# Performance work log

Measured on AMD Instinct MI355X. Metric: run time of the kernel, lower is better.

Reference implementation:

```python
import jax, jax.numpy as jnp
import numpy as np

B, S, DQK, DV, H = 4, 2048, 128, 128, 8


def setup_inputs() -> dict:
    key = jax.random.key(0)
    ks = jax.random.split(key, 9)
    s = 0.02
    return {
        "query": jax.random.normal(ks[0], (B, S, DQK), jnp.float32),
        "key": jax.random.normal(ks[1], (B, S, DQK), jnp.float32),
        "value": jax.random.normal(ks[2], (B, S, DV), jnp.float32),
        "WQ": jax.random.normal(ks[3], (DQK, H * DQK), jnp.float32) * s,
        "bQ": jax.random.normal(ks[4], (H * DQK,), jnp.float32) * s,
        "WK": jax.random.normal(ks[5], (DQK, H * DQK), jnp.float32) * s,
        "bK": jax.random.normal(ks[6], (H * DQK,), jnp.float32) * s,
        "WV": jax.random.normal(ks[7], (DV, H * DV), jnp.float32) * s,
        "bV": jax.random.normal(ks[8], (H * DV,), jnp.float32) * s,
    }


def reference(query, key, value, WQ, bQ, WK, bK, WV, bV):
    b, qn, dqk = query.shape
    kn = key.shape[1]
    dv = value.shape[2]
    h = H
    # projections -> [b, n, h, d]
    Q = (query @ WQ + bQ).reshape(b, qn, h, dqk)
    K = (key @ WK + bK).reshape(b, kn, h, dqk)
    V = (value @ WV + bV).reshape(b, kn, h, dv)
    # abs(QK^T)/sqrt(dk) score -- non-standard, prevents flash kernels
    scores = jnp.abs(jnp.einsum("bqhd,bkhd->bhqk", Q, K)) / jnp.sqrt(
        jnp.asarray(dqk, query.dtype)
    )
    w = jax.nn.softmax(scores, axis=-1)  # [b,h,q,k]
    # (complex cast +0j in the original is numerically a no-op on real V)
    out = jnp.einsum("bhqk,bkhd->bqhd", w, V).reshape(b, qn, h * dv)
    return out
```

## Files before the change

kernel.cpp:

```cpp
#include <hip/hip_runtime.h>
#include <hip/hip_bf16.h>

#define B_ 4
#define S_ 2048
#define D_ 128
#define H_ 8

typedef __attribute__((ext_vector_type(8))) short bf16x8;
typedef __attribute__((ext_vector_type(4))) float f32x4;

__device__ __forceinline__ short f2bf(float f) {
  union { float f; unsigned u; } v; v.f = f;
  unsigned u = v.u;
  unsigned r = (u + 0x7FFFu + ((u >> 16) & 1u)) >> 16;
  return (short)r;
}

__device__ __forceinline__ short4 pack4(f32x4 p) {
  union { __hip_bfloat162 h2[2]; short4 s4; } u;
  u.h2[0] = __float22bfloat162_rn(make_float2(p[0], p[1]));
  u.h2[1] = __float22bfloat162_rn(make_float2(p[2], p[3]));
  return u.s4;
}

__device__ __forceinline__ void dma16(const short* g, short* l) {
  __builtin_amdgcn_global_load_lds(
      (const __attribute__((address_space(1))) unsigned int*)g,
      (__attribute__((address_space(3))) unsigned int*)l, 16, 0, 0);
}

__global__ __launch_bounds__(256) void prep(
    const float* __restrict__ WQ, const float* __restrict__ WK, const float* __restrict__ WV,
    short* __restrict__ FQ, short* __restrict__ FK, short* __restrict__ FV) {
  __shared__ float tile[64][65];
  int bw = blockIdx.x >> 5;
  int tl = blockIdx.x & 31;
  int n0 = (tl & 15) * 64, k0 = (tl >> 4) * 64;
  const float* W = (bw == 0) ? WQ : (bw == 1) ? WK : WV;
  short* WF = (bw == 0) ? FQ : (bw == 1) ? FK : FV;
#pragma unroll
  for (int i = 0; i < 16; ++i) {
    int cix = threadIdx.x + 256 * i;
    int rr = cix >> 6, cc = cix & 63;
    tile[rr][cc] = W[(k0 + rr) * 1024 + n0 + cc];
  }
  __syncthreads();
#pragma unroll
  for (int i = 0; i < 16; ++i) {
    int cix = threadIdx.x + 256 * i;
    int rr = cix >> 6, cc = cix & 63;
    int n = n0 + rr, k = k0 + cc;
    size_t off = (size_t)(n >> 7) * 16384
               + (size_t)(((n >> 4) & 7) * 4 + (k >> 5)) * 512
               + ((k >> 3) & 3) * 128 + (n & 15) * 8 + (k & 7);
    WF[off] = f2bf(tile[cc][rr]);
  }
}

template <int MODE>
__device__ __forceinline__ void proj_pair(const float* __restrict__ X,
                                          const short* __restrict__ WF,
                                          const float* __restrict__ bias,
                                          short* __restrict__ out,
                                          int mtile, int np, short* sA) {
  int tid = threadIdx.x;
  int lane = tid & 63, w = tid >> 6;
  int l15 = lane & 15, l4 = lane >> 4;
  int m0 = mtile * 128;
  int bb = m0 >> 11;
  int mloc = m0 & 2047;

#pragma unroll
  for (int j = 0; j < 8; ++j) {
    int f = w * 8 + j;
    const float* src = X + (size_t)(m0 + (f >> 2) * 16 + l15) * 128 + (f & 3) * 32 + l4 * 8;
    float4 v0 = *(const float4*)src;
    float4 v1 = *(const float4*)(src + 4);
    union { struct { short4 lo, hi; } s; bf16x8 v; } u;
    u.s.lo = pack4((f32x4){v0.x, v0.y, v0.z, v0.w});
    u.s.hi = pack4((f32x4){v1.x, v1.y, v1.z, v1.w});
    *(bf16x8*)(sA + f * 512 + lane * 8) = u.v;
  }

  int wr = w >> 1, wc = w & 1;

  __syncthreads();

  bf16x8 a[4][4];
#pragma unroll
  for (int mi = 0; mi < 4; ++mi)
#pragma unroll
    for (int st = 0; st < 4; ++st)
      a[mi][st] = *(const bf16x8*)(sA + ((wr * 4 + mi) * 4 + st) * 512 + lane * 8);

#pragma unroll
  for (int nt = 0; nt < 2; ++nt) {
    int ntile = np * 2 + nt;
    int n0 = ntile * 128;

    const short* wfb = WF + (size_t)ntile * 16384 + wc * 8192 + lane * 8;

    f32x4 acc[4][4];
#pragma unroll
    for (int mi = 0; mi < 4; ++mi)
#pragma unroll
      for (int ni = 0; ni < 4; ++ni) acc[mi][ni] = (f32x4){0.f, 0.f, 0.f, 0.f};

#pragma unroll
    for (int ni = 0; ni < 4; ++ni) {
      bf16x8 bfr[4];
#pragma unroll
      for (int st = 0; st < 4; ++st)
        bfr[st] = *(const bf16x8*)(wfb + (ni * 4 + st) * 512);
#pragma unroll
      for (int mi = 0; mi < 4; ++mi) {
#pragma unroll
        for (int st = 0; st < 4; ++st) {
          if (MODE <= 1)
            acc[mi][ni] = __builtin_amdgcn_mfma_f32_16x16x32_bf16(bfr[st], a[mi][st], acc[mi][ni], 0, 0, 0);
          else
            acc[mi][ni] = __builtin_amdgcn_mfma_f32_16x16x32_bf16(a[mi][st], bfr[st], acc[mi][ni], 0, 0, 0);
        }
      }
    }

    __syncthreads();

    if (MODE == 0) {
#pragma unroll
      for (int mi = 0; mi < 4; ++mi) {
        int lrow = wr * 64 + mi * 16 + l15;
#pragma unroll
        for (int ni = 0; ni < 4; ++ni) {
          int d0 = wc * 64 + ni * 16 + l4 * 4;
          float4 bv = *(const float4*)(bias + n0 + d0);
          f32x4 t = acc[mi][ni];
          t[0] += bv.x; t[1] += bv.y; t[2] += bv.z; t[3] += bv.w;
          *(short4*)(sA + lrow * 128 + d0) = pack4(t);
        }
      }
    } else if (MODE == 1) {
#pragma unroll
      for (int mi = 0; mi < 4; ++mi) {
        int lk = wr * 64 + mi * 16 + l15;
        int kbase = (lk >> 6) * 8192 + ((lk >> 4) & 3) * 2048 + (lk & 15) * 8;
#pragma unroll
        for (int ni = 0; ni < 4; ++ni) {
          int d0 = wc * 64 + ni * 16 + l4 * 4;
          float4 bv = *(const float4*)(bias + n0 + d0);
          f32x4 t = acc[mi][ni];
          t[0] += bv.x; t[1] += bv.y; t[2] += bv.z; t[3] += bv.w;
          *(short4*)(sA + kbase + (d0 >> 5) * 512 + ((d0 >> 3) & 3) * 128 + (d0 & 7)) = pack4(t);
        }
      }
    } else {
#pragma unroll
      for (int ni = 0; ni < 4; ++ni) {
        int d = wc * 64 + ni * 16 + l15;
        float bvs = bias[n0 + d];
#pragma unroll
        for (int mi = 0; mi < 4; ++mi) {
          int ls0 = wr * 64 + mi * 16 + l4 * 4;
          f32x4 t = acc[mi][ni];
          t[0] += bvs; t[1] += bvs; t[2] += bvs; t[3] += bvs;
          *(short4*)(sA + (ls0 >> 6) * 8192
                        + ((d >> 4) * 2 + ((ls0 >> 5) & 1)) * 512
                        + ((ls0 >> 3) & 3) * 128 + (d & 15) * 8
                        + (ls0 & 7)) = pack4(t);
        }
      }
    }
    __syncthreads();

    short* gdst;
    if (MODE == 0)
      gdst = out + ((size_t)(bb * H_ + ntile) * S_ + mloc) * D_;
    else
      gdst = out + (size_t)(bb * H_ + ntile) * (S_ * D_) + (size_t)(mloc >> 6) * 8192;
#pragma unroll
    for (int i = 0; i < 8; ++i) {
      bf16x8 vv = *(const bf16x8*)(sA + (i * 256 + tid) * 8);
      *(bf16x8*)(gdst + (i * 256 + tid) * 8) = vv;
    }
  }
}

__global__ __launch_bounds__(256, 3) void proj3(
    const float* __restrict__ xq, const float* __restrict__ xk, const float* __restrict__ xv,
    const short* __restrict__ wtq, const short* __restrict__ wtk, const short* __restrict__ wtv,
    const float* __restrict__ bQ, const float* __restrict__ bK, const float* __restrict__ bV,
    short* __restrict__ Qp, short* __restrict__ Kf, short* __restrict__ Vf) {
  __shared__ short sA[16384];
  int work = (blockIdx.x & 7) * 96 + (blockIdx.x >> 3);
  int which = work >> 8;
  int t = work & 255;
  int mtile = t >> 2, np = t & 3;
  if (which == 0)      proj_pair<0>(xq, wtq, bQ, Qp, mtile, np, sA);
  else if (which == 1) proj_pair<1>(xk, wtk, bK, Kf, mtile, np, sA);
  else                 proj_pair<2>(xv, wtv, bV, Vf, mtile, np, sA);
}

#define PSTR 72

#define QK_H(KR)                                                               \
  _Pragma("unroll") for (int m = 0; m < 2; ++m) {                              \
    s0[m] = (f32x4){0.f, 0.f, 0.f, 0.f};                                       \
    s1[m] = (f32x4){0.f, 0.f, 0.f, 0.f};                                       \
    _Pragma("unroll") for (int st = 0; st < 4; ++st) {                         \
      s0[m] = __builtin_amdgcn_mfma_f32_16x16x32_bf16(KR[m * 4 + st], aq[0][st], s0[m], 0, 0, 0); \
      s1[m] = __builtin_amdgcn_mfma_f32_16x16x32_bf16(KR[m * 4 + st], aq[1][st], s1[m], 0, 0, 0); \
    }                                                                          \
  }

#define SM_H()                                                                 \
  _Pragma("unroll") for (int m = 0; m < 2; ++m) {                              \
    _Pragma("unroll") for (int r = 0; r < 4; ++r) {                            \
      float p = __builtin_amdgcn_exp2f(fabsf(s0[m][r]) * SC2);                 \
      ls0 += p;                                                                \
      s0[m][r] = p;                                                            \
    }                                                                          \
    *(short4*)(pw0 + l15 * PSTR + m * 16 + l4 * 4) = pack4(s0[m]);             \
  }                                                                            \
  _Pragma("unroll") for (int m = 0; m < 2; ++m) {                              \
    _Pragma("unroll") for (int r = 0; r < 4; ++r) {                            \
      float p = __builtin_amdgcn_exp2f(fabsf(s1[m][r]) * SC2);                 \
      ls1 += p;                                                                \
      s1[m][r] = p;                                                            \
    }                                                                          \
    *(short4*)(pw1 + l15 * PSTR + m * 16 + l4 * 4) = pack4(s1[m]);             \
  }                                                                            \
  ap0 = *(const bf16x8*)(pw0 + l15 * PSTR + l4 * 8);                           \
  ap1 = *(const bf16x8*)(pw1 + l15 * PSTR + l4 * 8);

#define PV_H()                                                                 \
  _Pragma("unroll") for (int t8 = 0; t8 < 8; ++t8) {                           \
    o0[t8] = __builtin_amdgcn_mfma_f32_16x16x32_bf16(ap0, bv[t8], o0[t8], 0, 0, 0); \
    o1[t8] = __builtin_amdgcn_mfma_f32_16x16x32_bf16(ap1, bv[t8], o1[t8], 0, 0, 0); \
  }

__global__ __launch_bounds__(512, 2) void attn(const short* __restrict__ Qp,
                                               const short* __restrict__ Kf,
                                               const short* __restrict__ Vf,
                                               float* __restrict__ out) {
  __shared__ short sK0[8192], sK1[8192];
  __shared__ short sV0[8192], sV1[8192];
  __shared__ short sP[16 * 16 * PSTR];

  int tid = threadIdx.x;
  int lane = tid & 63, w = tid >> 6;
  int xcd = blockIdx.x & 7;
  int idx = blockIdx.x >> 3;
  int bh  = xcd * 4 + (idx & 3);
  int qt  = idx >> 2;
  int q0  = qt * 256;
  int l15 = lane & 15, l4 = lane >> 4;

  const short* Qbase = Qp + (size_t)bh * S_ * D_;
  const short* kgs = Kf + (size_t)bh * S_ * D_ + 2 * w * 512 + lane * 8;
  const short* vgs = Vf + (size_t)bh * S_ * D_ + 2 * w * 512 + lane * 8;

  dma16(kgs,       sK0 + 2 * w * 512);
  dma16(kgs + 512, sK0 + (2 * w + 1) * 512);
  dma16(vgs,       sV0 + 2 * w * 512);
  dma16(vgs + 512, sV0 + (2 * w + 1) * 512);

  bf16x8 aq[2][4];
#pragma unroll
  for (int g = 0; g < 2; ++g)
#pragma unroll
    for (int st = 0; st < 4; ++st)
      aq[g][st] = *(const bf16x8*)(Qbase + (q0 + w * 32 + g * 16 + l15) * D_ + l4 * 8 + 32 * st);

  f32x4 o0[8], o1[8];
#pragma unroll
  for (int t = 0; t < 8; ++t) {
    o0[t] = (f32x4){0.f, 0.f, 0.f, 0.f};
    o1[t] = (f32x4){0.f, 0.f, 0.f, 0.f};
  }
  float ls0 = 0.f, ls1 = 0.f;

  const float SC2 = 0.127530637f;
  short* pw0 = sP + w * 16 * PSTR;
  short* pw1 = sP + (8 + w) * 16 * PSTR;

  __syncthreads();

  for (int t = 0; t < 32; ++t) {
    const short* sKc = (t & 1) ? sK1 : sK0;
    const short* sVc = (t & 1) ? sV1 : sV0;
    if (t < 31) {
      short* sKn = (t & 1) ? sK0 : sK1;
      short* sVn = (t & 1) ? sV0 : sV1;
      const short* kn = kgs + (size_t)(t + 1) * 8192;
      const short* vn = vgs + (size_t)(t + 1) * 8192;
      dma16(kn,       sKn + 2 * w * 512);
      dma16(kn + 512, sKn + (2 * w + 1) * 512);
      dma16(vn,       sVn + 2 * w * 512);
      dma16(vn + 512, sVn + (2 * w + 1) * 512);
    }
    bf16x8 kA[8], kB[8], bv[8];
#pragma unroll
    for (int j = 0; j < 8; ++j)
      kA[j] = *(const bf16x8*)(sKc + j * 512 + lane * 8);
#pragma unroll
    for (int j = 0; j < 8; ++j)
      kB[j] = *(const bf16x8*)(sKc + 4096 + j * 512 + lane * 8);
#pragma unroll
    for (int j = 0; j < 8; ++j)
      bv[j] = *(const bf16x8*)(sVc + (2 * j) * 512 + lane * 8);
    __builtin_amdgcn_sched_barrier(0);

    f32x4 s0[2], s1[2];
    bf16x8 ap0, ap1;
    __builtin_amdgcn_s_setprio(1);
    QK_H(kA);
    __builtin_amdgcn_s_setprio(0);
    SM_H();
    __builtin_amdgcn_s_setprio(1);
    PV_H();
    __builtin_amdgcn_s_setprio(0);
#pragma unroll
    for (int j = 0; j < 8; ++j)
      bv[j] = *(const bf16x8*)(sVc + (2 * j + 1) * 512 + lane * 8);
    __builtin_amdgcn_s_setprio(1);
    QK_H(kB);
    __builtin_amdgcn_s_setprio(0);
    SM_H();
    __builtin_amdgcn_s_setprio(1);
    PV_H();
    __builtin_amdgcn_s_setprio(0);
    __syncthreads();
  }

  ls0 += __shfl_xor(ls0, 16);
  ls0 += __shfl_xor(ls0, 32);
  ls1 += __shfl_xor(ls1, 16);
  ls1 += __shfl_xor(ls1, 32);
  float inv0[4], inv1[4];
#pragma unroll
  for (int r = 0; r < 4; ++r) {
    inv0[r] = 1.f / __shfl(ls0, l4 * 4 + r);
    inv1[r] = 1.f / __shfl(ls1, l4 * 4 + r);
  }

  int bb = bh >> 3, h = bh & 7;
#pragma unroll
  for (int t = 0; t < 8; ++t) {
#pragma unroll
    for (int r = 0; r < 4; ++r) {
      int qA = q0 + w * 32 + l4 * 4 + r;
      int qB = qA + 16;
      out[((size_t)(bb * S_ + qA)) * (H_ * D_) + h * D_ + t * 16 + l15] = o0[t][r] * inv0[r];
      out[((size_t)(bb * S_ + qB)) * (H_ * D_) + h * D_ + t * 16 + l15] = o1[t][r] * inv1[r];
    }
  }
}

extern "C" void kernel_launch(void* const* d_in, const int* in_sizes, int n_in,
                              void* d_out, int out_size, void* d_ws, size_t ws_size,
                              hipStream_t stream) {
  (void)in_sizes; (void)n_in; (void)out_size; (void)ws_size;
  const float* q  = (const float*)d_in[0];
  const float* k  = (const float*)d_in[1];
  const float* v  = (const float*)d_in[2];
  const float* WQ = (const float*)d_in[3];
  const float* bQ = (const float*)d_in[4];
  const float* WK = (const float*)d_in[5];
  const float* bK = (const float*)d_in[6];
  const float* WV = (const float*)d_in[7];
  const float* bV = (const float*)d_in[8];

  const int NW = D_ * H_ * D_;
  const int NP = B_ * H_ * S_ * D_;

  short* ws  = (short*)d_ws;
  short* wtq = ws;
  short* wtk = wtq + NW;
  short* wtv = wtk + NW;
  short* Qp  = wtv + NW;
  short* Kf  = Qp + NP;
  short* Vf  = Kf + NP;

  prep<<<96, 256, 0, stream>>>(WQ, WK, WV, wtq, wtk, wtv);

  proj3<<<768, 256, 0, stream>>>(q, k, v, wtq, wtk, wtv, bQ, bK, bV, Qp, Kf, Vf);

  attn<<<256, 512, 0, stream>>>(Qp, Kf, Vf, (float*)d_out);
}
```

Baseline: 176.2 us.

## Transpose softmax P tile via lane shuffles and halve attention block size

The probability tile is now rearranged from the MFMA accumulator layout into the A-operand layout with cross-lane shuffles, replacing the round trip through a shared-memory staging buffer. The attention kernel also moves to 256-thread blocks covering 128 queries each, launching twice as many blocks, with each wave issuing twice as many K/V DMA copies per tile. This removes LDS traffic and the shared P buffer and lowers per-block LDS use, but adds shuffle instructions and doubles total K/V loads across blocks.

```diff
diff --git a/kernel.cpp b/kernel.cpp
--- a/kernel.cpp
+++ b/kernel.cpp
@@ -200,8 +200,6 @@
   else                 proj_pair<2>(xv, wtv, bV, Vf, mtile, np, sA);
 }
 
-#define PSTR 72
-
 #define QK_H(KR)                                                               \
   _Pragma("unroll") for (int m = 0; m < 2; ++m) {                              \
     s0[m] = (f32x4){0.f, 0.f, 0.f, 0.f};                                       \
@@ -212,25 +210,30 @@
     }                                                                          \
   }
 
-#define SM_H()                                                                 \
-  _Pragma("unroll") for (int m = 0; m < 2; ++m) {                              \
-    _Pragma("unroll") for (int r = 0; r < 4; ++r) {                            \
-      float p = __builtin_amdgcn_exp2f(fabsf(s0[m][r]) * SC2);                 \
-      ls0 += p;                                                                \
-      s0[m][r] = p;                                                            \
+#define SM_X(S, LS, AP)                                                        \
+  {                                                                            \
+    _Pragma("unroll") for (int m = 0; m < 2; ++m) {                            \
+      _Pragma("unroll") for (int r = 0; r < 4; ++r) {                          \
+        float p = __builtin_amdgcn_exp2f(fabsf(S[m][r]) * SC2);                \
+        LS += p;                                                               \
+        S[m][r] = p;                                                           \
+      }                                                                        \
     }                                                                          \
-    *(short4*)(pw0 + l15 * PSTR + m * 16 + l4 * 4) = pack4(s0[m]);             \
-  }                                                                            \
-  _Pragma("unroll") for (int m = 0; m < 2; ++m) {                              \
-    _Pragma("unroll") for (int r = 0; r < 4; ++r) {                            \
-      float p = __builtin_amdgcn_exp2f(fabsf(s1[m][r]) * SC2);                 \
-      ls1 += p;                                                                \
-      s1[m][r] = p;                                                            \
-    }                                                                          \
-    *(short4*)(pw1 + l15 * PSTR + m * 16 + l4 * 4) = pack4(s1[m]);             \
-  }                                                                            \
-  ap0 = *(const bf16x8*)(pw0 + l15 * PSTR + l4 * 8);                           \
-  ap1 = *(const bf16x8*)(pw1 + l15 * PSTR + l4 * 8);
+    short4 pk0_ = pack4(S[0]);                                                 \
+    short4 pk1_ = pack4(S[1]);                                                 \
+    int X0_ = ((int2*)&pk0_)->x, X1_ = ((int2*)&pk0_)->y;                      \
+    int X2_ = ((int2*)&pk1_)->x, X3_ = ((int2*)&pk1_)->y;                      \
+    int A0_ = __shfl(X0_, sb), B0_ = __shfl(X2_, sb);                          \
+    int A1_ = __shfl(X1_, sb), B1_ = __shfl(X3_, sb);                          \
+    int A2_ = __shfl(X0_, sb + 16), B2_ = __shfl(X2_, sb + 16);                \
+    int A3_ = __shfl(X1_, sb + 16), B3_ = __shfl(X3_, sb + 16);                \
+    union { int u[4]; bf16x8 v; } uu_;                                         \
+    uu_.u[0] = hi_ ? B0_ : A0_;                                                \
+    uu_.u[1] = hi_ ? B1_ : A1_;                                                \
+    uu_.u[2] = hi_ ? B2_ : A2_;                                                \
+    uu_.u[3] = hi_ ? B3_ : A3_;                                                \
+    AP = uu_.v;                                                                \
+  }
 
 #define PV_H()                                                                 \
   _Pragma("unroll") for (int t8 = 0; t8 < 8; ++t8) {                           \
@@ -238,13 +241,12 @@
     o1[t8] = __builtin_amdgcn_mfma_f32_16x16x32_bf16(ap1, bv[t8], o1[t8], 0, 0, 0); \
   }
 
-__global__ __launch_bounds__(512, 2) void attn(const short* __restrict__ Qp,
+__global__ __launch_bounds__(256, 2) void attn(const short* __restrict__ Qp,
                                                const short* __restrict__ Kf,
                                                const short* __restrict__ Vf,
                                                float* __restrict__ out) {
   __shared__ short sK0[8192], sK1[8192];
   __shared__ short sV0[8192], sV1[8192];
-  __shared__ short sP[16 * 16 * PSTR];
 
   int tid = threadIdx.x;
   int lane = tid & 63, w = tid >> 6;
@@ -252,17 +254,24 @@
   int idx = blockIdx.x >> 3;
   int bh  = xcd * 4 + (idx & 3);
   int qt  = idx >> 2;
-  int q0  = qt * 256;
+  int q0  = qt * 128;
   int l15 = lane & 15, l4 = lane >> 4;
 
+  int sb = l15 + ((lane & 16) << 1);
+  bool hi_ = (lane >= 32);
+
   const short* Qbase = Qp + (size_t)bh * S_ * D_;
-  const short* kgs = Kf + (size_t)bh * S_ * D_ + 2 * w * 512 + lane * 8;
-  const short* vgs = Vf + (size_t)bh * S_ * D_ + 2 * w * 512 + lane * 8;
-
-  dma16(kgs,       sK0 + 2 * w * 512);
-  dma16(kgs + 512, sK0 + (2 * w + 1) * 512);
-  dma16(vgs,       sV0 + 2 * w * 512);
-  dma16(vgs + 512, sV0 + (2 * w + 1) * 512);
+  const short* kgs = Kf + (size_t)bh * S_ * D_ + 4 * w * 512 + lane * 8;
+  const short* vgs = Vf + (size_t)bh * S_ * D_ + 4 * w * 512 + lane * 8;
+
+  dma16(kgs,        sK0 + 4 * w * 512);
+  dma16(kgs + 512,  sK0 + (4 * w + 1) * 512);
+  dma16(kgs + 1024, sK0 + (4 * w + 2) * 512);
+  dma16(kgs + 1536, sK0 + (4 * w + 3) * 512);
+  dma16(vgs,        sV0 + 4 * w * 512);
+  dma16(vgs + 512,  sV0 + (4 * w + 1) * 512);
+  dma16(vgs + 1024, sV0 + (4 * w + 2) * 512);
+  dma16(vgs + 1536, sV0 + (4 * w + 3) * 512);
 
   bf16x8 aq[2][4];
 #pragma unroll
@@ -280,8 +289,6 @@
   float ls0 = 0.f, ls1 = 0.f;
 
   const float SC2 = 0.127530637f;
-  short* pw0 = sP + w * 16 * PSTR;
-  short* pw1 = sP + (8 + w) * 16 * PSTR;
 
   __syncthreads();
 
@@ -293,10 +300,14 @@
       short* sVn = (t & 1) ? sV0 : sV1;
       const short* kn = kgs + (size_t)(t + 1) * 8192;
       const short* vn = vgs + (size_t)(t + 1) * 8192;
-      dma16(kn,       sKn + 2 * w * 512);
-      dma16(kn + 512, sKn + (2 * w + 1) * 512);
-      dma16(vn,       sVn + 2 * w * 512);
-      dma16(vn + 512, sVn + (2 * w + 1) * 512);
+      dma16(kn,        sKn + 4 * w * 512);
+      dma16(kn + 512,  sKn + (4 * w + 1) * 512);
+      dma16(kn + 1024, sKn + (4 * w + 2) * 512);
+      dma16(kn + 1536, sKn + (4 * w + 3) * 512);
+      dma16(vn,        sVn + 4 * w * 512);
+      dma16(vn + 512,  sVn + (4 * w + 1) * 512);
+      dma16(vn + 1024, sVn + (4 * w + 2) * 512);
+      dma16(vn + 1536, sVn + (4 * w + 3) * 512);
     }
     bf16x8 kA[8], kB[8], bv[8];
 #pragma unroll
@@ -315,7 +326,8 @@
     __builtin_amdgcn_s_setprio(1);
     QK_H(kA);
     __builtin_amdgcn_s_setprio(0);
-    SM_H();
+    SM_X(s0, ls0, ap0);
+    SM_X(s1, ls1, ap1);
     __builtin_amdgcn_s_setprio(1);
     PV_H();
     __builtin_amdgcn_s_setprio(0);
@@ -325,7 +337,8 @@
     __builtin_amdgcn_s_setprio(1);
     QK_H(kB);
     __builtin_amdgcn_s_setprio(0);
-    SM_H();
+    SM_X(s0, ls0, ap0);
+    SM_X(s1, ls1, ap1);
     __builtin_amdgcn_s_setprio(1);
     PV_H();
     __builtin_amdgcn_s_setprio(0);
@@ -385,5 +398,5 @@
 
   proj3<<<768, 256, 0, stream>>>(q, k, v, wtq, wtk, wtv, bQ, bK, bV, Qp, Kf, Vf);
 
-  attn<<<256, 512, 0, stream>>>(Qp, Kf, Vf, (float*)d_out);
-}
+  attn<<<512, 256, 0, stream>>>(Qp, Kf, Vf, (float*)d_out);
+}
```

Result: slower. 192.8 us (+9.4%).
